# Performance work log

Hardware: AMD Instinct MI355X
Metric: run time of the kernel (lower is better)

## Reference

```python
import jax, jax.numpy as jnp
import numpy as np

B = 4096       # batch
S = 4096       # seq_len == input_dim
DEPTH = 2
D_MODEL = 1
D_FFN = 2      # d_model * d_ffn_factor
EPS = 1e-5


def _layernorm(x, w, b):
    mu = jnp.mean(x, axis=-1, keepdims=True)
    var = jnp.mean((x - mu) ** 2, axis=-1, keepdims=True)
    return (x - mu) * jax.lax.rsqrt(var + EPS) * w + b


def setup_inputs() -> dict:
    key = jax.random.key(0)
    ks = jax.random.split(key, 16)
    sc = lambda fan_in: 1.0 / np.sqrt(fan_in)
    inp = {
        "x": jax.random.normal(ks[0], (B, S), dtype=jnp.float32),
        # per-depth stacked gMLP block params
        "ln1_w": jnp.ones((DEPTH, D_MODEL), jnp.float32),
        "ln1_b": jnp.zeros((DEPTH, D_MODEL), jnp.float32),
        "cp1_w": jax.random.uniform(ks[1], (DEPTH, D_FFN, D_MODEL), jnp.float32, -sc(D_MODEL), sc(D_MODEL)),
        "cp1_b": jax.random.uniform(ks[2], (DEPTH, D_FFN), jnp.float32, -sc(D_MODEL), sc(D_MODEL)),
        "sgu_ln_w": jnp.ones((DEPTH, D_FFN // 2), jnp.float32),
        "sgu_ln_b": jnp.zeros((DEPTH, D_FFN // 2), jnp.float32),
        "sgu_proj_w": jax.random.uniform(ks[3], (DEPTH, S, S), jnp.float32, -sc(S), sc(S)),
        "sgu_proj_b": jax.random.uniform(ks[4], (DEPTH, S), jnp.float32, -sc(S), sc(S)),
        "cp2_w": jax.random.uniform(ks[5], (DEPTH, D_MODEL, D_FFN // 2), jnp.float32, -sc(D_FFN // 2), sc(D_FFN // 2)),
        "cp2_b": jax.random.uniform(ks[6], (DEPTH, D_MODEL), jnp.float32, -sc(D_FFN // 2), sc(D_FFN // 2)),
        "pooler_w": jax.random.uniform(ks[7], (S, S), jnp.float32, -sc(S), sc(S)),
        "pooler_b": jax.random.uniform(ks[8], (S,), jnp.float32, -sc(S), sc(S)),
        "cls_w": jax.random.uniform(ks[9], (1, S), jnp.float32, -sc(S), sc(S)),
        "cls_b": jax.random.uniform(ks[10], (1,), jnp.float32, -sc(S), sc(S)),
    }
    return inp


def reference(x, ln1_w, ln1_b, cp1_w, cp1_b, sgu_ln_w, sgu_ln_b,
              sgu_proj_w, sgu_proj_b, cp2_w, cp2_b,
              pooler_w, pooler_b, cls_w, cls_b):
    gelu = lambda t: jax.nn.gelu(t, approximate=False)
    h = x[..., None]                                   # [B, S, 1]
    for i in range(DEPTH):
        res = h
        t = _layernorm(h, ln1_w[i], ln1_b[i])          # [B, S, 1]
        t = gelu(t @ cp1_w[i].T + cp1_b[i])            # [B, S, 2]
        u, v = t[..., :D_FFN // 2], t[..., D_FFN // 2:]
        v = _layernorm(v, sgu_ln_w[i], sgu_ln_b[i])
        # transpose(1,2) -> Linear(S,S) -> transpose back, fused as einsum
        v = jnp.einsum('st,btc->bsc', sgu_proj_w[i], v) + sgu_proj_b[i][:, None]
        h = u * v                                      # [B, S, 1]
        h = h @ cp2_w[i].T + cp2_b[i] + res            # [B, S, 1]
    out = h[..., 0]                                    # [B, S]
    out = gelu(out @ pooler_w.T + pooler_b)            # [B, S]
    logits = out @ cls_w.T + cls_b                     # [B, 1]
    return logits[..., 0]                              # [B]
```

## Files before the change

kernel.cpp:

```cpp
#include <hip/hip_runtime.h>


#define K_DIM 4096

typedef __bf16 bf16x8 __attribute__((ext_vector_type(8)));
typedef float f32x4 __attribute__((ext_vector_type(4)));

__device__ __forceinline__ ushort f2bf(float f) {
    unsigned int u = __float_as_uint(f);
    u = (u + 0x7fffu + ((u >> 16) & 1u)) >> 16;
    return (ushort)u;
}

__device__ __forceinline__ float gelu_exact(float x) {
    return 0.5f * x * (1.0f + erff(x * 0.70710678118654752440f));
}

__device__ __forceinline__ void gld16(const void* g, void* l) {
    __builtin_amdgcn_global_load_lds(
        (__attribute__((address_space(1))) void*)(g),
        (__attribute__((address_space(3))) void*)(l), 16, 0, 0);
}

__global__ __launch_bounds__(256) void cvt2_kernel(const float* __restrict__ s0,
                                                   ushort* __restrict__ d0,
                                                   const float* __restrict__ s1,
                                                   ushort* __restrict__ d1) {
    int b = blockIdx.x;
    const float* src = (b < 8192) ? s0 : s1;
    ushort* dst = (b < 8192) ? d0 : d1;
    int i = (b & 8191) * 256 + threadIdx.x;
    const float4* s4 = (const float4*)src + (size_t)i * 2;
    float4 a = s4[0], c = s4[1];
    union { ushort u[8]; uint4 v; } r;
    r.u[0] = f2bf(a.x); r.u[1] = f2bf(a.y); r.u[2] = f2bf(a.z); r.u[3] = f2bf(a.w);
    r.u[4] = f2bf(c.x); r.u[5] = f2bf(c.y); r.u[6] = f2bf(c.z); r.u[7] = f2bf(c.w);
    ((uint4*)dst)[i] = r.v;
}

__global__ __launch_bounds__(256) void rowsum_kernel(const float* __restrict__ proj_w,
                                                     const float* __restrict__ sgu_ln_b,
                                                     float* __restrict__ R) {
    int wid  = (blockIdx.x * 256 + threadIdx.x) >> 6;
    int lane = threadIdx.x & 63;
    int layer = wid >> 12;
    float beta = sgu_ln_b[layer];
    if (beta == 0.0f) {
        if (lane == 0) R[wid] = 0.0f;
        return;
    }
    const float* pr = proj_w + (size_t)wid * K_DIM;
    float s = 0.0f;
    for (int it = 0; it < 16; ++it) {
        float4 pv = *(const float4*)&pr[it * 256 + lane * 4];
        s += pv.x + pv.y + pv.z + pv.w;
    }
#pragma unroll
    for (int m = 1; m < 64; m <<= 1) s += __shfl_xor(s, m);
    if (lane == 0) R[wid] = s;
}

__global__ __launch_bounds__(256) void c_kernel(const float* __restrict__ ln1_b,
                                                const float* __restrict__ cp1_w,
                                                const float* __restrict__ cp1_b,
                                                const float* __restrict__ sgu_ln_b,
                                                const float* __restrict__ sgu_proj_b,
                                                const float* __restrict__ cp2_w,
                                                const float* __restrict__ cp2_b,
                                                const float* __restrict__ cls_b,
                                                const float* __restrict__ R,
                                                float* __restrict__ c,
                                                float* __restrict__ out) {
    int t = blockIdx.x * 256 + threadIdx.x;
    float cv = 0.0f;
#pragma unroll
    for (int i = 0; i < 2; ++i) {
        float alpha = gelu_exact(ln1_b[i] * cp1_w[i * 2 + 0] + cp1_b[i * 2 + 0]);
        float beta  = sgu_ln_b[i];
        float v     = beta * R[i * 4096 + t] + sgu_proj_b[i * 4096 + t];
        cv += alpha * v * cp2_w[i] + cp2_b[i];
    }
    c[t]   = cv;
    out[t] = cls_b[0];
}

__global__ __launch_bounds__(256) void e_kernel(const ushort* __restrict__ Pb,
                                                const float* __restrict__ c,
                                                const float* __restrict__ pooler_b,
                                                float* __restrict__ e) {
    int row  = blockIdx.x * 4 + (threadIdx.x >> 6);
    int lane = threadIdx.x & 63;
    const ushort* pr = Pb + (size_t)row * K_DIM;
    float s = 0.0f;
    for (int it = 0; it < 8; ++it) {
        int col = it * 512 + lane * 8;
        bf16x8 pv = *(const bf16x8*)&pr[col];
#pragma unroll
        for (int j = 0; j < 8; ++j) s += (float)pv[j] * c[col + j];
    }
#pragma unroll
    for (int m = 1; m < 64; m <<= 1) s += __shfl_xor(s, m);
    if (lane == 0) e[row] = s + pooler_b[row];
}

__global__ __launch_bounds__(256, 2) void gemm_kernel(const ushort* __restrict__ X,
                                                      const ushort* __restrict__ P,
                                                      const float* __restrict__ clsW,
                                                      const float* __restrict__ e,
                                                      float* __restrict__ accOut) {
    __shared__ __align__(16) ushort As[256 * 64];
    __shared__ __align__(16) ushort Bs[128 * 64];

    const int t = threadIdx.x;
    const int bCol = blockIdx.x, bRow = blockIdx.y;
    const int lane = t & 63, wv = t >> 6;
    const int g = lane >> 4, lo = lane & 15;
    const int wm = wv >> 1, wn = wv & 1;

    f32x4 zero4 = {0.f, 0.f, 0.f, 0.f};
    f32x4 acc[8][4];
#pragma unroll
    for (int mi = 0; mi < 8; ++mi)
#pragma unroll
        for (int ni = 0; ni < 4; ++ni) acc[mi][ni] = zero4;

    const int sr = t >> 3;
    const int cs = (t & 7) ^ (sr & 7);
    const ushort* gA = X + (size_t)(bRow * 256 + sr) * K_DIM + cs * 8;
    const ushort* gB = P + (size_t)(bCol * 128 + sr) * K_DIM + cs * 8;
    char* lA = (char*)As + t * 16;
    char* lB = (char*)Bs + t * 16;

    for (int k0 = 0; k0 < K_DIM; k0 += 64) {
#pragma unroll
        for (int rd = 0; rd < 8; ++rd)
            gld16(gA + (size_t)(rd * 32) * K_DIM, lA + rd * 4096);
#pragma unroll
        for (int rd = 0; rd < 4; ++rd)
            gld16(gB + (size_t)(rd * 32) * K_DIM, lB + rd * 4096);
        gA += 64;
        gB += 64;
        __syncthreads();

#pragma unroll
        for (int kk = 0; kk < 2; ++kk) {
            const int ch = (((kk << 2) | g) ^ (lo & 7)) * 8;
            bf16x8 af[8], bfr[4];
#pragma unroll
            for (int mi = 0; mi < 8; ++mi) {
                int row = wm * 128 + mi * 16 + lo;
                af[mi] = *(const bf16x8*)&As[row * 64 + ch];
            }
#pragma unroll
            for (int ni = 0; ni < 4; ++ni) {
                int col = wn * 64 + ni * 16 + lo;
                bfr[ni] = *(const bf16x8*)&Bs[col * 64 + ch];
            }
#pragma unroll
            for (int mi = 0; mi < 8; ++mi)
#pragma unroll
                for (int ni = 0; ni < 4; ++ni)
                    acc[mi][ni] = __builtin_amdgcn_mfma_f32_16x16x32_bf16(af[mi], bfr[ni], acc[mi][ni], 0, 0, 0);
        }
        __syncthreads();
    }

    int sColBase = bCol * 128 + wn * 64 + lo;
    float eb[4], cw[4];
#pragma unroll
    for (int ni = 0; ni < 4; ++ni) {
        int s = sColBase + ni * 16;
        eb[ni] = e[s];
        cw[ni] = clsW[s];
    }
#pragma unroll
    for (int mi = 0; mi < 8; ++mi) {
        int rowBase = bRow * 256 + wm * 128 + mi * 16 + g * 4;
#pragma unroll
        for (int r = 0; r < 4; ++r) {
            float sum = 0.0f;
#pragma unroll
            for (int ni = 0; ni < 4; ++ni) {
                float y = acc[mi][ni][r] + eb[ni];
                sum += gelu_exact(y) * cw[ni];
            }
            sum += __shfl_xor(sum, 1);
            sum += __shfl_xor(sum, 2);
            sum += __shfl_xor(sum, 4);
            sum += __shfl_xor(sum, 8);
            if (lo == 0) atomicAdd(&accOut[rowBase + r], sum);
        }
    }
}

extern "C" void kernel_launch(void* const* d_in, const int* in_sizes, int n_in,
                              void* d_out, int out_size, void* d_ws, size_t ws_size,
                              hipStream_t stream) {
    const float* x          = (const float*)d_in[0];
    const float* ln1_b      = (const float*)d_in[2];
    const float* cp1_w      = (const float*)d_in[3];
    const float* cp1_b      = (const float*)d_in[4];
    const float* sgu_ln_b   = (const float*)d_in[6];
    const float* sgu_proj_w = (const float*)d_in[7];
    const float* sgu_proj_b = (const float*)d_in[8];
    const float* cp2_w      = (const float*)d_in[9];
    const float* cp2_b      = (const float*)d_in[10];
    const float* pooler_w   = (const float*)d_in[11];
    const float* pooler_b   = (const float*)d_in[12];
    const float* cls_w      = (const float*)d_in[13];
    const float* cls_b      = (const float*)d_in[14];

    ushort* xb = (ushort*)d_ws;
    ushort* pb = xb + (size_t)K_DIM * K_DIM;
    float*  fs = (float*)(pb + (size_t)K_DIM * K_DIM);
    float* c_buf = fs;
    float* e_buf = fs + 4096;
    float* R     = fs + 8192;
    float* out   = (float*)d_out;

    cvt2_kernel<<<16384, 256, 0, stream>>>(x, xb, pooler_w, pb);
    rowsum_kernel<<<2048, 256, 0, stream>>>(sgu_proj_w, sgu_ln_b, R);
    c_kernel<<<16, 256, 0, stream>>>(ln1_b, cp1_w, cp1_b, sgu_ln_b, sgu_proj_b,
                                     cp2_w, cp2_b, cls_b, R, c_buf, out);
    e_kernel<<<1024, 256, 0, stream>>>(pb, c_buf, pooler_b, e_buf);
    gemm_kernel<<<dim3(32, 16), 256, 0, stream>>>(xb, pb, cls_w, e_buf, out);
}
```

Measured before the change: 399.2 us.

## Double-buffer GEMM with 256x256 tiles, fuse e-vector into conversion, fold rowsum

The GEMM moves to 512-thread blocks with 256x256 output tiles and double-buffered LDS, using manual waitcnt/barrier scheduling, a swizzled block order and raised MFMA priority. The e = P·c product is now computed inside the bf16 conversion kernel with per-wave atomics, which removes a separate pass over the converted pooler weight. The projection row-sum moves into c_kernel and is skipped when the SGU LayerNorm bias is zero. The atomics add contention, and the reordered fp32 sums may shift numerics slightly.

```diff
diff --git a/kernel.cpp b/kernel.cpp
--- a/kernel.cpp
+++ b/kernel.cpp
@@ -22,54 +22,18 @@
         (__attribute__((address_space(3))) void*)(l), 16, 0, 0);
 }
 
-__global__ __launch_bounds__(256) void cvt2_kernel(const float* __restrict__ s0,
-                                                   ushort* __restrict__ d0,
-                                                   const float* __restrict__ s1,
-                                                   ushort* __restrict__ d1) {
-    int b = blockIdx.x;
-    const float* src = (b < 8192) ? s0 : s1;
-    ushort* dst = (b < 8192) ? d0 : d1;
-    int i = (b & 8191) * 256 + threadIdx.x;
-    const float4* s4 = (const float4*)src + (size_t)i * 2;
-    float4 a = s4[0], c = s4[1];
-    union { ushort u[8]; uint4 v; } r;
-    r.u[0] = f2bf(a.x); r.u[1] = f2bf(a.y); r.u[2] = f2bf(a.z); r.u[3] = f2bf(a.w);
-    r.u[4] = f2bf(c.x); r.u[5] = f2bf(c.y); r.u[6] = f2bf(c.z); r.u[7] = f2bf(c.w);
-    ((uint4*)dst)[i] = r.v;
-}
-
-__global__ __launch_bounds__(256) void rowsum_kernel(const float* __restrict__ proj_w,
-                                                     const float* __restrict__ sgu_ln_b,
-                                                     float* __restrict__ R) {
-    int wid  = (blockIdx.x * 256 + threadIdx.x) >> 6;
-    int lane = threadIdx.x & 63;
-    int layer = wid >> 12;
-    float beta = sgu_ln_b[layer];
-    if (beta == 0.0f) {
-        if (lane == 0) R[wid] = 0.0f;
-        return;
-    }
-    const float* pr = proj_w + (size_t)wid * K_DIM;
-    float s = 0.0f;
-    for (int it = 0; it < 16; ++it) {
-        float4 pv = *(const float4*)&pr[it * 256 + lane * 4];
-        s += pv.x + pv.y + pv.z + pv.w;
-    }
-#pragma unroll
-    for (int m = 1; m < 64; m <<= 1) s += __shfl_xor(s, m);
-    if (lane == 0) R[wid] = s;
-}
-
 __global__ __launch_bounds__(256) void c_kernel(const float* __restrict__ ln1_b,
                                                 const float* __restrict__ cp1_w,
                                                 const float* __restrict__ cp1_b,
                                                 const float* __restrict__ sgu_ln_b,
+                                                const float* __restrict__ sgu_proj_w,
                                                 const float* __restrict__ sgu_proj_b,
                                                 const float* __restrict__ cp2_w,
                                                 const float* __restrict__ cp2_b,
                                                 const float* __restrict__ cls_b,
-                                                const float* __restrict__ R,
+                                                const float* __restrict__ pooler_b,
                                                 float* __restrict__ c,
+                                                float* __restrict__ e,
                                                 float* __restrict__ out) {
     int t = blockIdx.x * 256 + threadIdx.x;
     float cv = 0.0f;
@@ -77,45 +41,65 @@
     for (int i = 0; i < 2; ++i) {
         float alpha = gelu_exact(ln1_b[i] * cp1_w[i * 2 + 0] + cp1_b[i * 2 + 0]);
         float beta  = sgu_ln_b[i];
-        float v     = beta * R[i * 4096 + t] + sgu_proj_b[i * 4096 + t];
+        float Ri = 0.0f;
+        if (beta != 0.0f) {
+            const float* pr = sgu_proj_w + ((size_t)i * 4096 + t) * K_DIM;
+            for (int k = 0; k < K_DIM; k += 4) {
+                float4 pv = *(const float4*)&pr[k];
+                Ri += pv.x + pv.y + pv.z + pv.w;
+            }
+        }
+        float v = beta * Ri + sgu_proj_b[i * 4096 + t];
         cv += alpha * v * cp2_w[i] + cp2_b[i];
     }
     c[t]   = cv;
+    e[t]   = pooler_b[t];
     out[t] = cls_b[0];
 }
 
-__global__ __launch_bounds__(256) void e_kernel(const ushort* __restrict__ Pb,
-                                                const float* __restrict__ c,
-                                                const float* __restrict__ pooler_b,
-                                                float* __restrict__ e) {
-    int row  = blockIdx.x * 4 + (threadIdx.x >> 6);
-    int lane = threadIdx.x & 63;
-    const ushort* pr = Pb + (size_t)row * K_DIM;
-    float s = 0.0f;
-    for (int it = 0; it < 8; ++it) {
-        int col = it * 512 + lane * 8;
-        bf16x8 pv = *(const bf16x8*)&pr[col];
-#pragma unroll
-        for (int j = 0; j < 8; ++j) s += (float)pv[j] * c[col + j];
-    }
-#pragma unroll
-    for (int m = 1; m < 64; m <<= 1) s += __shfl_xor(s, m);
-    if (lane == 0) e[row] = s + pooler_b[row];
-}
-
-__global__ __launch_bounds__(256, 2) void gemm_kernel(const ushort* __restrict__ X,
+__global__ __launch_bounds__(256) void cvt2_kernel(const float* __restrict__ s0,
+                                                   ushort* __restrict__ d0,
+                                                   const float* __restrict__ s1,
+                                                   ushort* __restrict__ d1,
+                                                   const float* __restrict__ c,
+                                                   float* __restrict__ e) {
+    int b = blockIdx.x;
+    bool isP = (b >= 8192);
+    const float* src = isP ? s1 : s0;
+    ushort* dst = isP ? d1 : d0;
+    int i = (b & 8191) * 256 + threadIdx.x;
+    const float4* s4 = (const float4*)src + (size_t)i * 2;
+    float4 a = s4[0], q = s4[1];
+    union { ushort u[8]; uint4 v; } r;
+    r.u[0] = f2bf(a.x); r.u[1] = f2bf(a.y); r.u[2] = f2bf(a.z); r.u[3] = f2bf(a.w);
+    r.u[4] = f2bf(q.x); r.u[5] = f2bf(q.y); r.u[6] = f2bf(q.z); r.u[7] = f2bf(q.w);
+    ((uint4*)dst)[i] = r.v;
+    if (isP) {
+        int col = (i << 3) & 4095;
+        float s = a.x * c[col + 0] + a.y * c[col + 1] + a.z * c[col + 2] + a.w * c[col + 3]
+                + q.x * c[col + 4] + q.y * c[col + 5] + q.z * c[col + 6] + q.w * c[col + 7];
+#pragma unroll
+        for (int m = 1; m < 64; m <<= 1) s += __shfl_xor(s, m);
+        if ((threadIdx.x & 63) == 0) atomicAdd(&e[i >> 9], s);
+    }
+}
+
+__global__ __launch_bounds__(512, 2) void gemm_kernel(const ushort* __restrict__ X,
                                                       const ushort* __restrict__ P,
                                                       const float* __restrict__ clsW,
                                                       const float* __restrict__ e,
                                                       float* __restrict__ accOut) {
-    __shared__ __align__(16) ushort As[256 * 64];
-    __shared__ __align__(16) ushort Bs[128 * 64];
+    __shared__ __align__(16) ushort As[2][256 * 64];
+    __shared__ __align__(16) ushort Bs[2][256 * 64];
 
     const int t = threadIdx.x;
-    const int bCol = blockIdx.x, bRow = blockIdx.y;
+    const int flat = blockIdx.x;
+    const int swz = (flat & 7) * 32 + (flat >> 3);
+    const int bRow = swz >> 4, bCol = swz & 15;
+
     const int lane = t & 63, wv = t >> 6;
     const int g = lane >> 4, lo = lane & 15;
-    const int wm = wv >> 1, wn = wv & 1;
+    const int wm = wv >> 2, wn = wv & 3;
 
     f32x4 zero4 = {0.f, 0.f, 0.f, 0.f};
     f32x4 acc[8][4];
@@ -127,45 +111,59 @@
     const int sr = t >> 3;
     const int cs = (t & 7) ^ (sr & 7);
     const ushort* gA = X + (size_t)(bRow * 256 + sr) * K_DIM + cs * 8;
-    const ushort* gB = P + (size_t)(bCol * 128 + sr) * K_DIM + cs * 8;
-    char* lA = (char*)As + t * 16;
-    char* lB = (char*)Bs + t * 16;
-
-    for (int k0 = 0; k0 < K_DIM; k0 += 64) {
-#pragma unroll
-        for (int rd = 0; rd < 8; ++rd)
-            gld16(gA + (size_t)(rd * 32) * K_DIM, lA + rd * 4096);
-#pragma unroll
-        for (int rd = 0; rd < 4; ++rd)
-            gld16(gB + (size_t)(rd * 32) * K_DIM, lB + rd * 4096);
-        gA += 64;
-        gB += 64;
-        __syncthreads();
-
-#pragma unroll
-        for (int kk = 0; kk < 2; ++kk) {
-            const int ch = (((kk << 2) | g) ^ (lo & 7)) * 8;
-            bf16x8 af[8], bfr[4];
-#pragma unroll
-            for (int mi = 0; mi < 8; ++mi) {
-                int row = wm * 128 + mi * 16 + lo;
-                af[mi] = *(const bf16x8*)&As[row * 64 + ch];
-            }
-#pragma unroll
-            for (int ni = 0; ni < 4; ++ni) {
-                int col = wn * 64 + ni * 16 + lo;
-                bfr[ni] = *(const bf16x8*)&Bs[col * 64 + ch];
-            }
-#pragma unroll
-            for (int mi = 0; mi < 8; ++mi)
-#pragma unroll
-                for (int ni = 0; ni < 4; ++ni)
-                    acc[mi][ni] = __builtin_amdgcn_mfma_f32_16x16x32_bf16(af[mi], bfr[ni], acc[mi][ni], 0, 0, 0);
-        }
-        __syncthreads();
-    }
-
-    int sColBase = bCol * 128 + wn * 64 + lo;
+    const ushort* gB = P + (size_t)(bCol * 256 + sr) * K_DIM + cs * 8;
+    char* lA0 = (char*)&As[0][0] + t * 16;
+    char* lB0 = (char*)&Bs[0][0] + t * 16;
+
+#define STAGE(buf, k0)                                                            \
+    do {                                                                          \
+        _Pragma("unroll") for (int r_ = 0; r_ < 4; ++r_)                          \
+            gld16(gA + (size_t)(r_ * 64) * K_DIM + (k0), lA0 + (buf)*32768 + r_ * 8192); \
+        _Pragma("unroll") for (int r_ = 0; r_ < 4; ++r_)                          \
+            gld16(gB + (size_t)(r_ * 64) * K_DIM + (k0), lB0 + (buf)*32768 + r_ * 8192); \
+    } while (0)
+
+#define COMPUTE(buf)                                                              \
+    do {                                                                          \
+        _Pragma("unroll") for (int kk = 0; kk < 2; ++kk) {                        \
+            const int ch = (((kk << 2) | g) ^ (lo & 7)) << 3;                     \
+            bf16x8 af[8], bfr[4];                                                 \
+            _Pragma("unroll") for (int mi = 0; mi < 8; ++mi)                      \
+                af[mi] = *(const bf16x8*)&As[buf][(wm * 128 + mi * 16 + lo) * 64 + ch]; \
+            _Pragma("unroll") for (int ni = 0; ni < 4; ++ni)                      \
+                bfr[ni] = *(const bf16x8*)&Bs[buf][(wn * 64 + ni * 16 + lo) * 64 + ch]; \
+            __builtin_amdgcn_s_setprio(1);                                        \
+            _Pragma("unroll") for (int mi = 0; mi < 8; ++mi)                      \
+                _Pragma("unroll") for (int ni = 0; ni < 4; ++ni)                  \
+                    acc[mi][ni] = __builtin_amdgcn_mfma_f32_16x16x32_bf16(        \
+                        af[mi], bfr[ni], acc[mi][ni], 0, 0, 0);                   \
+            __builtin_amdgcn_s_setprio(0);                                        \
+        }                                                                         \
+    } while (0)
+
+    STAGE(0, 0);
+#pragma unroll 1
+    for (int k0 = 64; k0 < 3968; k0 += 128) {
+        STAGE(1, k0);
+        asm volatile("s_waitcnt vmcnt(8)\n\ts_barrier" ::: "memory");
+        COMPUTE(0);
+        asm volatile("s_barrier" ::: "memory");
+        STAGE(0, k0 + 64);
+        asm volatile("s_waitcnt vmcnt(8)\n\ts_barrier" ::: "memory");
+        COMPUTE(1);
+        asm volatile("s_barrier" ::: "memory");
+    }
+    STAGE(1, 4032);
+    asm volatile("s_waitcnt vmcnt(8)\n\ts_barrier" ::: "memory");
+    COMPUTE(0);
+    asm volatile("s_barrier" ::: "memory");
+    asm volatile("s_waitcnt vmcnt(0)\n\ts_barrier" ::: "memory");
+    COMPUTE(1);
+
+#undef STAGE
+#undef COMPUTE
+
+    int sColBase = bCol * 256 + wn * 64 + lo;
     float eb[4], cw[4];
 #pragma unroll
     for (int ni = 0; ni < 4; ++ni) {
@@ -215,13 +213,11 @@
     float*  fs = (float*)(pb + (size_t)K_DIM * K_DIM);
     float* c_buf = fs;
     float* e_buf = fs + 4096;
-    float* R     = fs + 8192;
     float* out   = (float*)d_out;
 
-    cvt2_kernel<<<16384, 256, 0, stream>>>(x, xb, pooler_w, pb);
-    rowsum_kernel<<<2048, 256, 0, stream>>>(sgu_proj_w, sgu_ln_b, R);
-    c_kernel<<<16, 256, 0, stream>>>(ln1_b, cp1_w, cp1_b, sgu_ln_b, sgu_proj_b,
-                                     cp2_w, cp2_b, cls_b, R, c_buf, out);
-    e_kernel<<<1024, 256, 0, stream>>>(pb, c_buf, pooler_b, e_buf);
-    gemm_kernel<<<dim3(32, 16), 256, 0, stream>>>(xb, pb, cls_w, e_buf, out);
-}
+    c_kernel<<<16, 256, 0, stream>>>(ln1_b, cp1_w, cp1_b, sgu_ln_b, sgu_proj_w,
+                                     sgu_proj_b, cp2_w, cp2_b, cls_b, pooler_b,
+                                     c_buf, e_buf, out);
+    cvt2_kernel<<<16384, 256, 0, stream>>>(x, xb, pooler_w, pb, c_buf, e_buf);
+    gemm_kernel<<<256, 512, 0, stream>>>(xb, pb, cls_w, e_buf, out);
+}
```

Measured after the change: 410.0 us. +2.7%, slower.
